# Performance work log

Hardware: AMD Instinct MI355X
Metric: run time of the kernel (lower is better)

Reference implementation:

```python
import jax, jax.numpy as jnp
import numpy as np

B, T, C = 4, 2048, 2048
N_HEAD = 16
HEAD_DIM = C // N_HEAD  # 128


def _apply_rotary_emb(x, cos, sin):
    # x: (B, T, H, D), cos/sin: (1, T, 1, D/2)
    d = x.shape[-1] // 2
    x1, x2 = x[..., :d], x[..., d:]
    return jnp.concatenate([x1 * cos + x2 * sin, -x2 * sin + x1 * cos], axis=-1)


def setup_inputs() -> dict:
    key = jax.random.key(0)
    ks = jax.random.split(key, 7)
    s = 0.02
    return {
        "x": jax.random.normal(ks[0], (B, T, C), dtype=jnp.float32),
        "cos": jax.random.normal(ks[1], (1, T, 1, HEAD_DIM // 2), dtype=jnp.float32),
        "sin": jax.random.normal(ks[2], (1, T, 1, HEAD_DIM // 2), dtype=jnp.float32),
        "wq": jax.random.normal(ks[3], (C, C), dtype=jnp.float32) * s,
        "wk": jax.random.normal(ks[4], (C, C), dtype=jnp.float32) * s,
        "wv": jax.random.normal(ks[5], (C, C), dtype=jnp.float32) * s,
        "wo": jax.random.normal(ks[6], (C, C), dtype=jnp.float32) * s,
    }


def reference(x, cos, sin, wq, wk, wv, wo):
    b, t, c = x.shape
    h, d = N_HEAD, HEAD_DIM
    # linear projections (torch Linear: x @ W.T), reshape to (B, T, H, D)
    q = (x @ wq.T).reshape(b, t, h, d)
    k = (x @ wk.T).reshape(b, t, h, d)
    v = (x @ wv.T).reshape(b, t, h, d)
    q = _apply_rotary_emb(q, cos, sin)
    k = _apply_rotary_emb(k, cos, sin)
    # scaled dot-product attention, non-causal; heads on axis 2
    scale = 1.0 / jnp.sqrt(jnp.float32(d))
    scores = jnp.einsum("bqhd,bkhd->bhqk", q, k) * scale
    attn = jax.nn.softmax(scores, axis=-1)
    y = jnp.einsum("bhqk,bkhd->bqhd", attn, v).reshape(b, t, c)
    return y @ wo.T
```

## Files before the change

### kernel.cpp

```cpp
#include <hip/hip_runtime.h>

#define B_SZ 4
#define T_SZ 2048
#define C_SZ 2048
#define H_SZ 16
#define D_SZ 128

typedef __attribute__((ext_vector_type(8))) __bf16 bf16x8;
typedef __attribute__((ext_vector_type(4))) float f32x4;
typedef __attribute__((ext_vector_type(4))) unsigned short us4;

static __device__ __forceinline__ unsigned short f2bf(float f) {
  unsigned u = __builtin_bit_cast(unsigned, f);
  u += 0x7fffu + ((u >> 16) & 1u);
  return (unsigned short)(u >> 16);
}

static __device__ __forceinline__ void gload16(const void* g, void* l) {
  __builtin_amdgcn_global_load_lds((__attribute__((address_space(1))) void*)(g),
                                   (__attribute__((address_space(3))) void*)(l), 16, 0, 0);
}

__global__ __launch_bounds__(256) void cast_f32_bf16(const float* __restrict__ src,
                                                     unsigned short* __restrict__ dst, int n4) {
  int i = blockIdx.x * 256 + threadIdx.x;
  if (i >= n4) return;
  float4 v = ((const float4*)src)[i];
  us4 o;
  o[0] = f2bf(v.x); o[1] = f2bf(v.y); o[2] = f2bf(v.z); o[3] = f2bf(v.w);
  ((us4*)dst)[i] = o;
}

template <int EPI>
__global__ __launch_bounds__(512, 2) void gemm_bt(const unsigned short* __restrict__ A,
                                                  const unsigned short* __restrict__ W,
                                                  void* __restrict__ out,
                                                  const float* __restrict__ cosp,
                                                  const float* __restrict__ sinp,
                                                  float outScale, int M, int N, int K) {
  __shared__ unsigned short As[2][256 * 64];
  __shared__ unsigned short Bs[2][256 * 64];
  const int tid = threadIdx.x;
  const int wave = tid >> 6, lane = tid & 63, quad = lane >> 4, l15 = lane & 15;
  const int wm = wave >> 1, wn = wave & 1;
  const int m0 = blockIdx.y * 256, n0 = blockIdx.x * 256;
  const int NT = K >> 6;

  const int srow = tid >> 3;
  const int kcol = ((tid & 7) ^ (srow & 7)) * 8;
  const unsigned short* aptr = A + (size_t)(m0 + srow) * K + kcol;
  const unsigned short* bptr = W + (size_t)(n0 + srow) * K + kcol;
  const int ldst = tid * 16;

#define STAGE(t)                                                                   \
  do {                                                                             \
    const int sl_ = (t) & 1;                                                       \
    const size_t kk_ = (size_t)(t) * 64;                                           \
    _Pragma("unroll") for (int j = 0; j < 4; ++j) {                                \
      gload16(aptr + (size_t)j * 64 * K + kk_, (char*)As[sl_] + j * 8192 + ldst);  \
      gload16(bptr + (size_t)j * 64 * K + kk_, (char*)Bs[sl_] + j * 8192 + ldst);  \
    }                                                                              \
  } while (0)

  f32x4 acc[4][8] = {};
  const int swz = l15 & 7;

  STAGE(0);
  for (int t = 0; t < NT; ++t) {
    if (t + 1 < NT) {
      STAGE(t + 1);
      asm volatile("s_waitcnt vmcnt(8)" ::: "memory");
    } else {
      asm volatile("s_waitcnt vmcnt(0)" ::: "memory");
    }
    __builtin_amdgcn_s_barrier();
    asm volatile("" ::: "memory");
    const unsigned short* Asl = As[t & 1];
    const unsigned short* Bsl = Bs[t & 1];
    bf16x8 af[4];
#pragma unroll
    for (int p = 0; p < 4; ++p) {
      const int ks = p >> 1, nh = p & 1;
      if (nh == 0) {
#pragma unroll
        for (int mf = 0; mf < 4; ++mf)
          af[mf] = *(const bf16x8*)&Asl[(wm * 64 + mf * 16 + l15) * 64 +
                                        (((ks * 4 + quad) ^ swz) * 8)];
      }
      bf16x8 bfr[4];
#pragma unroll
      for (int i = 0; i < 4; ++i)
        bfr[i] = *(const bf16x8*)&Bsl[(wn * 128 + (nh * 4 + i) * 16 + l15) * 64 +
                                      (((ks * 4 + quad) ^ swz) * 8)];
      __builtin_amdgcn_s_setprio(1);
#pragma unroll
      for (int i = 0; i < 4; ++i)
#pragma unroll
        for (int mf = 0; mf < 4; ++mf)
          acc[mf][nh * 4 + i] =
              __builtin_amdgcn_mfma_f32_16x16x32_bf16(af[mf], bfr[i], acc[mf][nh * 4 + i], 0, 0, 0);
      __builtin_amdgcn_s_setprio(0);
      __builtin_amdgcn_s_barrier();
      asm volatile("" ::: "memory");
    }
  }
#undef STAGE

  const int mb = m0 + wm * 64, nb = n0 + wn * 128;
  if (EPI == 1) {
    unsigned short* O = (unsigned short*)out;
#pragma unroll
    for (int mf = 0; mf < 4; ++mf)
#pragma unroll
      for (int r = 0; r < 4; ++r) {
        int m = mb + mf * 16 + quad * 4 + r;
        int tt = m & (T_SZ - 1);
#pragma unroll
        for (int nf = 0; nf < 4; ++nf) {
          int dd = nf * 16 + l15;
          float c = cosp[tt * 64 + dd];
          float s = sinp[tt * 64 + dd];
          float x1 = acc[mf][nf][r], x2 = acc[mf][nf + 4][r];
          O[(size_t)m * N + nb + dd]      = f2bf((x1 * c + x2 * s) * outScale);
          O[(size_t)m * N + nb + dd + 64] = f2bf((x1 * c - x2 * s) * outScale);
        }
      }
  } else if (EPI == 2) {
    unsigned short* O = (unsigned short*)out;
#pragma unroll
    for (int mf = 0; mf < 4; ++mf) {
      int m4 = mb + mf * 16 + quad * 4;
      int bb = m4 >> 11;
      int tt = m4 & (T_SZ - 1);
#pragma unroll
      for (int nf = 0; nf < 8; ++nf) {
        int n = nb + nf * 16 + l15;
        int h = n >> 7, d = n & (D_SZ - 1);
        us4 pk;
        pk[0] = f2bf(acc[mf][nf][0]);
        pk[1] = f2bf(acc[mf][nf][1]);
        pk[2] = f2bf(acc[mf][nf][2]);
        pk[3] = f2bf(acc[mf][nf][3]);
        *(us4*)&O[((size_t)((bb * H_SZ + h) * D_SZ + d)) * T_SZ + tt] = pk;
      }
    }
  } else {
    float* O = (float*)out;
#pragma unroll
    for (int mf = 0; mf < 4; ++mf)
#pragma unroll
      for (int nf = 0; nf < 8; ++nf)
#pragma unroll
        for (int r = 0; r < 4; ++r) {
          int m = mb + mf * 16 + quad * 4 + r;
          O[(size_t)m * N + nb + nf * 16 + l15] = acc[mf][nf][r];
        }
  }
}

static __device__ __forceinline__ void stage_kv(const unsigned short* __restrict__ Kg,
                                                const unsigned short* __restrict__ Vt,
                                                unsigned short* Kbuf, unsigned short* Vbuf,
                                                size_t kbase0, size_t vbase0, int kt, int tid) {
  size_t kb = kbase0 + (size_t)kt * 64 * C_SZ;
  size_t vb = vbase0 + (size_t)kt * 64;
#pragma unroll
  for (int s = 0; s < 4; ++s) {
    int ii = s * 256 + tid;
    int krow = ii >> 4, kpos = ii & 15, kc = kpos ^ (krow & 15);
    gload16(Kg + kb + (size_t)krow * C_SZ + kc * 8, (char*)Kbuf + ii * 16);
    int vrow = ii >> 3, vpos = ii & 7, vc = vpos ^ (vrow & 7);
    gload16(Vt + vb + (size_t)vrow * T_SZ + vc * 8, (char*)Vbuf + ii * 16);
  }
}

__global__ __launch_bounds__(256, 2) void attn_fused(const unsigned short* __restrict__ Q,
                                                     const unsigned short* __restrict__ Kg,
                                                     const unsigned short* __restrict__ Vt,
                                                     unsigned short* __restrict__ Y) {
  __shared__ unsigned short Ks[2][64 * 128];
  __shared__ unsigned short Vs[2][128 * 64];
  __shared__ unsigned short Ps[4][32 * 40];
  const int tid = threadIdx.x;
  const int wave = tid >> 6, lane = tid & 63, quad = lane >> 4, l15 = lane & 15;
  const int kh = wave & 1, qh = wave >> 1;
  const int qt = blockIdx.x, bh = blockIdx.y;
  const int b = bh >> 4, h = bh & 15;
  const float LOG2E = 1.44269504088896f;

  bf16x8 aq[2][4];
  {
    size_t qrow0 = (size_t)(b * T_SZ + qt * 64 + qh * 32);
#pragma unroll
    for (int nt = 0; nt < 2; ++nt)
#pragma unroll
      for (int ks = 0; ks < 4; ++ks)
        aq[nt][ks] = *(const bf16x8*)(Q + (qrow0 + nt * 16 + l15) * C_SZ + h * D_SZ + ks * 32 + quad * 8);
  }

  const size_t kbase0 = ((size_t)(b * T_SZ)) * C_SZ + h * D_SZ;
  const size_t vbase0 = ((size_t)(bh * D_SZ)) * T_SZ;
  stage_kv(Kg, Vt, Ks[0], Vs[0], kbase0, vbase0, 0, tid);
  stage_kv(Kg, Vt, Ks[1], Vs[1], kbase0, vbase0, 1, tid);

  float mstate[2] = {-1e30f, -1e30f}, lstate[2] = {0.f, 0.f};
  f32x4 o[8][2] = {};
  unsigned short* PsW = Ps[wave];
  __syncthreads();

  for (int jt = 0; jt < T_SZ / 128; ++jt) {
    bf16x8 bkA[2][4], bvA[8];
#pragma unroll
    for (int mt = 0; mt < 2; ++mt)
#pragma unroll
      for (int ks = 0; ks < 4; ++ks)
        bkA[mt][ks] = *(const bf16x8*)&Ks[0][(kh * 32 + mt * 16 + l15) * 128 + (((ks * 4 + quad) ^ l15) * 8)];
#pragma unroll
    for (int dt = 0; dt < 8; ++dt)
      bvA[dt] = *(const bf16x8*)&Vs[0][(dt * 16 + l15) * 64 + (((kh * 4 + quad) ^ (l15 & 7)) * 8)];
    f32x4 sfA[2][2] = {};
#pragma unroll
    for (int mt = 0; mt < 2; ++mt)
#pragma unroll
      for (int ks = 0; ks < 4; ++ks)
#pragma unroll
        for (int nt = 0; nt < 2; ++nt)
          sfA[mt][nt] = __builtin_amdgcn_mfma_f32_16x16x32_bf16(bkA[mt][ks], aq[nt][ks], sfA[mt][nt], 0, 0, 0);
    __syncthreads();
    if (jt + 1 < T_SZ / 128) stage_kv(Kg, Vt, Ks[0], Vs[0], kbase0, vbase0, 2 * jt + 2, tid);
    bf16x8 bkB[2][4], bvB[8];
#pragma unroll
    for (int mt = 0; mt < 2; ++mt)
#pragma unroll
      for (int ks = 0; ks < 4; ++ks)
        bkB[mt][ks] = *(const bf16x8*)&Ks[1][(kh * 32 + mt * 16 + l15) * 128 + (((ks * 4 + quad) ^ l15) * 8)];
#pragma unroll
    for (int dt = 0; dt < 8; ++dt)
      bvB[dt] = *(const bf16x8*)&Vs[1][(dt * 16 + l15) * 64 + (((kh * 4 + quad) ^ (l15 & 7)) * 8)];
    f32x4 sfB[2][2] = {};
#pragma unroll
    for (int mt = 0; mt < 2; ++mt)
#pragma unroll
      for (int ks = 0; ks < 4; ++ks)
#pragma unroll
        for (int nt = 0; nt < 2; ++nt)
          sfB[mt][nt] = __builtin_amdgcn_mfma_f32_16x16x32_bf16(bkB[mt][ks], aq[nt][ks], sfB[mt][nt], 0, 0, 0);
    float alpha[2], rsum[2];
#pragma unroll
    for (int nt = 0; nt < 2; ++nt) {
      float rmax = sfA[0][nt][0];
#pragma unroll
      for (int mt = 0; mt < 2; ++mt)
#pragma unroll
        for (int r = 0; r < 4; ++r) {
          rmax = fmaxf(rmax, sfA[mt][nt][r]);
          rmax = fmaxf(rmax, sfB[mt][nt][r]);
        }
      rmax = fmaxf(rmax, __shfl_xor(rmax, 16));
      rmax = fmaxf(rmax, __shfl_xor(rmax, 32));
      float mnew = fmaxf(mstate[nt], rmax);
      alpha[nt] = exp2f((mstate[nt] - mnew) * LOG2E);
      mstate[nt] = mnew;
      rsum[nt] = 0.f;
    }
#pragma unroll
    for (int dt = 0; dt < 8; ++dt)
#pragma unroll
      for (int nt = 0; nt < 2; ++nt)
        o[dt][nt] *= alpha[nt];
#pragma unroll
    for (int nt = 0; nt < 2; ++nt)
#pragma unroll
      for (int mt = 0; mt < 2; ++mt) {
        us4 pk;
        float p0 = exp2f((sfA[mt][nt][0] - mstate[nt]) * LOG2E);
        float p1 = exp2f((sfA[mt][nt][1] - mstate[nt]) * LOG2E);
        float p2 = exp2f((sfA[mt][nt][2] - mstate[nt]) * LOG2E);
        float p3 = exp2f((sfA[mt][nt][3] - mstate[nt]) * LOG2E);
        rsum[nt] += (p0 + p1) + (p2 + p3);
        pk[0] = f2bf(p0); pk[1] = f2bf(p1); pk[2] = f2bf(p2); pk[3] = f2bf(p3);
        *(us4*)&PsW[(nt * 16 + l15) * 40 + mt * 16 + quad * 4] = pk;
      }
    {
      bf16x8 ap[2];
#pragma unroll
      for (int nt = 0; nt < 2; ++nt)
        ap[nt] = *(const bf16x8*)&PsW[(nt * 16 + l15) * 40 + quad * 8];
#pragma unroll
      for (int dt = 0; dt < 8; ++dt)
#pragma unroll
        for (int nt = 0; nt < 2; ++nt)
          o[dt][nt] = __builtin_amdgcn_mfma_f32_16x16x32_bf16(bvA[dt], ap[nt], o[dt][nt], 0, 0, 0);
    }
    asm volatile("" ::: "memory");
#pragma unroll
    for (int nt = 0; nt < 2; ++nt)
#pragma unroll
      for (int mt = 0; mt < 2; ++mt) {
        us4 pk;
        float p0 = exp2f((sfB[mt][nt][0] - mstate[nt]) * LOG2E);
        float p1 = exp2f((sfB[mt][nt][1] - mstate[nt]) * LOG2E);
        float p2 = exp2f((sfB[mt][nt][2] - mstate[nt]) * LOG2E);
        float p3 = exp2f((sfB[mt][nt][3] - mstate[nt]) * LOG2E);
        rsum[nt] += (p0 + p1) + (p2 + p3);
        pk[0] = f2bf(p0); pk[1] = f2bf(p1); pk[2] = f2bf(p2); pk[3] = f2bf(p3);
        *(us4*)&PsW[(nt * 16 + l15) * 40 + mt * 16 + quad * 4] = pk;
      }
    {
      bf16x8 ap[2];
#pragma unroll
      for (int nt = 0; nt < 2; ++nt)
        ap[nt] = *(const bf16x8*)&PsW[(nt * 16 + l15) * 40 + quad * 8];
#pragma unroll
      for (int dt = 0; dt < 8; ++dt)
#pragma unroll
        for (int nt = 0; nt < 2; ++nt)
          o[dt][nt] = __builtin_amdgcn_mfma_f32_16x16x32_bf16(bvB[dt], ap[nt], o[dt][nt], 0, 0, 0);
    }
#pragma unroll
    for (int nt = 0; nt < 2; ++nt) {
      rsum[nt] += __shfl_xor(rsum[nt], 16);
      rsum[nt] += __shfl_xor(rsum[nt], 32);
      lstate[nt] = lstate[nt] * alpha[nt] + rsum[nt];
    }
    __syncthreads();
    if (jt + 1 < T_SZ / 128) stage_kv(Kg, Vt, Ks[1], Vs[1], kbase0, vbase0, 2 * jt + 3, tid);
  }

  float* Xch = (float*)Ks;
  float* st  = (float*)Vs;
  if (kh == 1) {
#pragma unroll
    for (int dt = 0; dt < 8; ++dt)
#pragma unroll
      for (int nt = 0; nt < 2; ++nt)
        *(f32x4*)&Xch[((qh * 16 + dt * 2 + nt) * 64 + lane) * 4] = o[dt][nt];
    if (quad == 0) {
#pragma unroll
      for (int nt = 0; nt < 2; ++nt) {
        int q = qh * 32 + nt * 16 + l15;
        st[q] = mstate[nt];
        st[64 + q] = lstate[nt];
      }
    }
  }
  __syncthreads();
  if (kh == 0) {
#pragma unroll
    for (int nt = 0; nt < 2; ++nt) {
      int q = qh * 32 + nt * 16 + l15;
      float m1 = st[q], l1 = st[64 + q];
      float M = fmaxf(mstate[nt], m1);
      float a0 = exp2f((mstate[nt] - M) * LOG2E);
      float a1 = exp2f((m1 - M) * LOG2E);
      float L = lstate[nt] * a0 + l1 * a1;
      float inv = 1.0f / L;
      size_t row = (size_t)(b * T_SZ + qt * 64) + q;
#pragma unroll
      for (int dt = 0; dt < 8; ++dt) {
        f32x4 o1 = *(const f32x4*)&Xch[((qh * 16 + dt * 2 + nt) * 64 + lane) * 4];
        us4 pk;
        pk[0] = f2bf((o[dt][nt][0] * a0 + o1[0] * a1) * inv);
        pk[1] = f2bf((o[dt][nt][1] * a0 + o1[1] * a1) * inv);
        pk[2] = f2bf((o[dt][nt][2] * a0 + o1[2] * a1) * inv);
        pk[3] = f2bf((o[dt][nt][3] * a0 + o1[3] * a1) * inv);
        *(us4*)&Y[row * C_SZ + h * D_SZ + dt * 16 + quad * 4] = pk;
      }
    }
  }
}

extern "C" void kernel_launch(void* const* d_in, const int* in_sizes, int n_in,
                              void* d_out, int out_size, void* d_ws, size_t ws_size,
                              hipStream_t stream) {
  (void)in_sizes; (void)n_in; (void)out_size; (void)ws_size;
  const float* x    = (const float*)d_in[0];
  const float* cosp = (const float*)d_in[1];
  const float* sinp = (const float*)d_in[2];
  const float* wq   = (const float*)d_in[3];
  const float* wk   = (const float*)d_in[4];
  const float* wv   = (const float*)d_in[5];
  const float* wo   = (const float*)d_in[6];
  float* out = (float*)d_out;

  const size_t XE = (size_t)B_SZ * T_SZ * C_SZ;
  const size_t WE = (size_t)C_SZ * C_SZ;
  unsigned short* Xb = (unsigned short*)d_ws;
  unsigned short* Qb = Xb + XE;
  unsigned short* Kb = Qb + XE;
  unsigned short* Vt = Kb + XE;
  unsigned short* Wb = Vt + XE;
  unsigned short* Y  = Xb;

  const int M = B_SZ * T_SZ, N = C_SZ, K = C_SZ;
  dim3 ggrid(N / 256, M / 256);
  int nbx = (int)(XE / 4 / 256);
  int nbw = (int)(WE / 4 / 256);
  const float qscale = 0.088388347648318447f;

  cast_f32_bf16<<<nbx, 256, 0, stream>>>(x, Xb, (int)(XE / 4));

  cast_f32_bf16<<<nbw, 256, 0, stream>>>(wq, Wb, (int)(WE / 4));
  gemm_bt<1><<<ggrid, 512, 0, stream>>>(Xb, Wb, Qb, cosp, sinp, qscale, M, N, K);

  cast_f32_bf16<<<nbw, 256, 0, stream>>>(wk, Wb, (int)(WE / 4));
  gemm_bt<1><<<ggrid, 512, 0, stream>>>(Xb, Wb, Kb, cosp, sinp, 1.0f, M, N, K);

  cast_f32_bf16<<<nbw, 256, 0, stream>>>(wv, Wb, (int)(WE / 4));
  gemm_bt<2><<<ggrid, 512, 0, stream>>>(Xb, Wb, Vt, nullptr, nullptr, 1.0f, M, N, K);

  attn_fused<<<dim3(T_SZ / 64, B_SZ * H_SZ), 256, 0, stream>>>(Qb, Kb, Vt, Y);

  cast_f32_bf16<<<nbw, 256, 0, stream>>>(wo, Wb, (int)(WE / 4));
  gemm_bt<3><<<ggrid, 512, 0, stream>>>(Y, Wb, out, nullptr, nullptr, 1.0f, M, N, K);
}
```

Before: 724.9 us.

## Drop K/V double buffering to raise attention occupancy to three blocks

Replaces the two-stage double-buffered K/V pipeline, which handled 128 keys per iteration, with a single LDS buffer that is loaded and consumed 64 keys at a time, with barriers before and after each load. All shared arrays are packed into one smaller SMEM block, and launch bounds are raised to allow three blocks per CU. The aim is to hide global-load latency through more resident blocks rather than in-block prefetch. The cost is that each block now stalls on every tile load, pays two barriers per tile, and has a tighter register budget.

```diff
diff --git a/kernel.cpp b/kernel.cpp
--- a/kernel.cpp
+++ b/kernel.cpp
@@ -174,13 +174,14 @@
   }
 }
 
-__global__ __launch_bounds__(256, 2) void attn_fused(const unsigned short* __restrict__ Q,
+__global__ __launch_bounds__(256, 3) void attn_fused(const unsigned short* __restrict__ Q,
                                                      const unsigned short* __restrict__ Kg,
                                                      const unsigned short* __restrict__ Vt,
                                                      unsigned short* __restrict__ Y) {
-  __shared__ unsigned short Ks[2][64 * 128];
-  __shared__ unsigned short Vs[2][128 * 64];
-  __shared__ unsigned short Ps[4][32 * 40];
+  __shared__ unsigned short SMEM[21504];
+  unsigned short* Ks = SMEM;
+  unsigned short* Vs = SMEM + 8192;
+  unsigned short* Ps = SMEM + 16384;
   const int tid = threadIdx.x;
   const int wave = tid >> 6, lane = tid & 63, quad = lane >> 4, l15 = lane & 15;
   const int kh = wave & 1, qh = wave >> 1;
@@ -200,62 +201,41 @@
 
   const size_t kbase0 = ((size_t)(b * T_SZ)) * C_SZ + h * D_SZ;
   const size_t vbase0 = ((size_t)(bh * D_SZ)) * T_SZ;
-  stage_kv(Kg, Vt, Ks[0], Vs[0], kbase0, vbase0, 0, tid);
-  stage_kv(Kg, Vt, Ks[1], Vs[1], kbase0, vbase0, 1, tid);
 
   float mstate[2] = {-1e30f, -1e30f}, lstate[2] = {0.f, 0.f};
   f32x4 o[8][2] = {};
-  unsigned short* PsW = Ps[wave];
-  __syncthreads();
-
-  for (int jt = 0; jt < T_SZ / 128; ++jt) {
-    bf16x8 bkA[2][4], bvA[8];
+  unsigned short* PsW = Ps + wave * (32 * 40);
+
+  for (int kt = 0; kt < T_SZ / 64; ++kt) {
+    __syncthreads();
+    stage_kv(Kg, Vt, Ks, Vs, kbase0, vbase0, kt, tid);
+    __syncthreads();
+    bf16x8 bk[2][4], bv[8];
 #pragma unroll
     for (int mt = 0; mt < 2; ++mt)
 #pragma unroll
       for (int ks = 0; ks < 4; ++ks)
-        bkA[mt][ks] = *(const bf16x8*)&Ks[0][(kh * 32 + mt * 16 + l15) * 128 + (((ks * 4 + quad) ^ l15) * 8)];
+        bk[mt][ks] = *(const bf16x8*)&Ks[(kh * 32 + mt * 16 + l15) * 128 + (((ks * 4 + quad) ^ l15) * 8)];
 #pragma unroll
     for (int dt = 0; dt < 8; ++dt)
-      bvA[dt] = *(const bf16x8*)&Vs[0][(dt * 16 + l15) * 64 + (((kh * 4 + quad) ^ (l15 & 7)) * 8)];
-    f32x4 sfA[2][2] = {};
+      bv[dt] = *(const bf16x8*)&Vs[(dt * 16 + l15) * 64 + (((kh * 4 + quad) ^ (l15 & 7)) * 8)];
+    f32x4 sf[2][2] = {};
 #pragma unroll
     for (int mt = 0; mt < 2; ++mt)
 #pragma unroll
       for (int ks = 0; ks < 4; ++ks)
 #pragma unroll
         for (int nt = 0; nt < 2; ++nt)
-          sfA[mt][nt] = __builtin_amdgcn_mfma_f32_16x16x32_bf16(bkA[mt][ks], aq[nt][ks], sfA[mt][nt], 0, 0, 0);
-    __syncthreads();
-    if (jt + 1 < T_SZ / 128) stage_kv(Kg, Vt, Ks[0], Vs[0], kbase0, vbase0, 2 * jt + 2, tid);
-    bf16x8 bkB[2][4], bvB[8];
-#pragma unroll
-    for (int mt = 0; mt < 2; ++mt)
-#pragma unroll
-      for (int ks = 0; ks < 4; ++ks)
-        bkB[mt][ks] = *(const bf16x8*)&Ks[1][(kh * 32 + mt * 16 + l15) * 128 + (((ks * 4 + quad) ^ l15) * 8)];
-#pragma unroll
-    for (int dt = 0; dt < 8; ++dt)
-      bvB[dt] = *(const bf16x8*)&Vs[1][(dt * 16 + l15) * 64 + (((kh * 4 + quad) ^ (l15 & 7)) * 8)];
-    f32x4 sfB[2][2] = {};
-#pragma unroll
-    for (int mt = 0; mt < 2; ++mt)
-#pragma unroll
-      for (int ks = 0; ks < 4; ++ks)
-#pragma unroll
-        for (int nt = 0; nt < 2; ++nt)
-          sfB[mt][nt] = __builtin_amdgcn_mfma_f32_16x16x32_bf16(bkB[mt][ks], aq[nt][ks], sfB[mt][nt], 0, 0, 0);
+          sf[mt][nt] = __builtin_amdgcn_mfma_f32_16x16x32_bf16(bk[mt][ks], aq[nt][ks], sf[mt][nt], 0, 0, 0);
     float alpha[2], rsum[2];
 #pragma unroll
     for (int nt = 0; nt < 2; ++nt) {
-      float rmax = sfA[0][nt][0];
+      float rmax = sf[0][nt][0];
 #pragma unroll
       for (int mt = 0; mt < 2; ++mt)
 #pragma unroll
-        for (int r = 0; r < 4; ++r) {
-          rmax = fmaxf(rmax, sfA[mt][nt][r]);
-          rmax = fmaxf(rmax, sfB[mt][nt][r]);
-        }
+        for (int r = 0; r < 4; ++r)
+          rmax = fmaxf(rmax, sf[mt][nt][r]);
       rmax = fmaxf(rmax, __shfl_xor(rmax, 16));
       rmax = fmaxf(rmax, __shfl_xor(rmax, 32));
       float mnew = fmaxf(mstate[nt], rmax);
@@ -273,10 +253,10 @@
 #pragma unroll
       for (int mt = 0; mt < 2; ++mt) {
         us4 pk;
-        float p0 = exp2f((sfA[mt][nt][0] - mstate[nt]) * LOG2E);
-        float p1 = exp2f((sfA[mt][nt][1] - mstate[nt]) * LOG2E);
-        float p2 = exp2f((sfA[mt][nt][2] - mstate[nt]) * LOG2E);
-        float p3 = exp2f((sfA[mt][nt][3] - mstate[nt]) * LOG2E);
+        float p0 = exp2f((sf[mt][nt][0] - mstate[nt]) * LOG2E);
+        float p1 = exp2f((sf[mt][nt][1] - mstate[nt]) * LOG2E);
+        float p2 = exp2f((sf[mt][nt][2] - mstate[nt]) * LOG2E);
+        float p3 = exp2f((sf[mt][nt][3] - mstate[nt]) * LOG2E);
         rsum[nt] += (p0 + p1) + (p2 + p3);
         pk[0] = f2bf(p0); pk[1] = f2bf(p1); pk[2] = f2bf(p2); pk[3] = f2bf(p3);
         *(us4*)&PsW[(nt * 16 + l15) * 40 + mt * 16 + quad * 4] = pk;
@@ -290,32 +270,7 @@
       for (int dt = 0; dt < 8; ++dt)
 #pragma unroll
         for (int nt = 0; nt < 2; ++nt)
-          o[dt][nt] = __builtin_amdgcn_mfma_f32_16x16x32_bf16(bvA[dt], ap[nt], o[dt][nt], 0, 0, 0);
-    }
-    asm volatile("" ::: "memory");
-#pragma unroll
-    for (int nt = 0; nt < 2; ++nt)
-#pragma unroll
-      for (int mt = 0; mt < 2; ++mt) {
-        us4 pk;
-        float p0 = exp2f((sfB[mt][nt][0] - mstate[nt]) * LOG2E);
-        float p1 = exp2f((sfB[mt][nt][1] - mstate[nt]) * LOG2E);
-        float p2 = exp2f((sfB[mt][nt][2] - mstate[nt]) * LOG2E);
-        float p3 = exp2f((sfB[mt][nt][3] - mstate[nt]) * LOG2E);
-        rsum[nt] += (p0 + p1) + (p2 + p3);
-        pk[0] = f2bf(p0); pk[1] = f2bf(p1); pk[2] = f2bf(p2); pk[3] = f2bf(p3);
-        *(us4*)&PsW[(nt * 16 + l15) * 40 + mt * 16 + quad * 4] = pk;
-      }
-    {
-      bf16x8 ap[2];
-#pragma unroll
-      for (int nt = 0; nt < 2; ++nt)
-        ap[nt] = *(const bf16x8*)&PsW[(nt * 16 + l15) * 40 + quad * 8];
-#pragma unroll
-      for (int dt = 0; dt < 8; ++dt)
-#pragma unroll
-        for (int nt = 0; nt < 2; ++nt)
-          o[dt][nt] = __builtin_amdgcn_mfma_f32_16x16x32_bf16(bvB[dt], ap[nt], o[dt][nt], 0, 0, 0);
+          o[dt][nt] = __builtin_amdgcn_mfma_f32_16x16x32_bf16(bv[dt], ap[nt], o[dt][nt], 0, 0, 0);
     }
 #pragma unroll
     for (int nt = 0; nt < 2; ++nt) {
@@ -323,12 +278,11 @@
       rsum[nt] += __shfl_xor(rsum[nt], 32);
       lstate[nt] = lstate[nt] * alpha[nt] + rsum[nt];
     }
-    __syncthreads();
-    if (jt + 1 < T_SZ / 128) stage_kv(Kg, Vt, Ks[1], Vs[1], kbase0, vbase0, 2 * jt + 3, tid);
-  }
-
-  float* Xch = (float*)Ks;
-  float* st  = (float*)Vs;
+  }
+
+  float* Xch = (float*)SMEM;
+  float* st  = (float*)(SMEM + 16384);
+  __syncthreads();
   if (kh == 1) {
 #pragma unroll
     for (int dt = 0; dt < 8; ++dt)
```

Result: slower. 881.3 us (+21.6%).
